# Kernel optimization log

Measured on AMD Instinct MI355X. Metric: run time of the kernel, lower is better.

Reference implementation:

```python
import jax, jax.numpy as jnp
import numpy as np

V, E, U, L = 50000, 512, 20, 9   # vocab, embed dim, user feats, labels
R, S, T = 64, 32, 50             # reviews, sentences/review, tokens/sentence
D = E + U                        # product-encoder input dim


def setup_inputs() -> dict:
    key = jax.random.key(0)
    ks = jax.random.split(key, 16)
    sc = lambda k, shape: (jax.random.normal(k, shape, jnp.float32) * 0.02)
    return {
        "inputs": jax.random.randint(ks[0], (R, S, T), 0, V),
        "user_feats": jax.random.normal(ks[1], (R, U), jnp.float32),
        "embedding": sc(ks[2], (V, E)),
        "w_sent": sc(ks[3], (E, E)), "b_sent": jnp.zeros((E,), jnp.float32),
        "w_rev": sc(ks[4], (E, E)),  "b_rev": jnp.zeros((E,), jnp.float32),
        "w_prod": sc(ks[5], (D, D)), "b_prod": jnp.zeros((D,), jnp.float32),
        "w_rff": sc(ks[6], (D, 1)),  "b_rff": jnp.zeros((1,), jnp.float32),
        "w_pff": sc(ks[7], (D, L)),  "b_pff": jnp.zeros((L,), jnp.float32),
        "user_w": jnp.ones((U,), jnp.float32),
    }


def _masked_mean(x, mask):
    # x: [..., N, F], mask: [..., N] -> [..., F]
    denom = jnp.maximum(mask.sum(-1, keepdims=True), 1.0)
    return (x * mask[..., None]).sum(-2) / denom


def reference(inputs, user_feats, embedding, w_sent, b_sent, w_rev, b_rev,
              w_prod, b_prod, w_rff, b_rff, w_pff, b_pff, user_w):
    dt = embedding.dtype
    tok_mask = (inputs != 0).astype(dt)                      # [R,S,T]
    emb = embedding[inputs]                                  # [R,S,T,E]
    # sentence encoder (DAN): masked mean over tokens + Linear + SELU
    sent_h = jax.nn.selu(_masked_mean(emb, tok_mask) @ w_sent + b_sent)   # [R,S,E]
    # review encoder: masked mean over sentences (r_mask = p.sum(-1) != 0)
    sent_mask = (inputs.sum(-1) != 0).astype(dt)             # [R,S]
    rev_h = jax.nn.selu(_masked_mean(sent_h, sent_mask) @ w_rev + b_rev)  # [R,E]
    # append L2-normalized user feats scaled by learned weights
    norm = jnp.sqrt((user_feats * user_feats).sum(-1, keepdims=True))
    uf = user_feats / jnp.maximum(norm, 1e-12) * user_w      # [R,U]
    p_batch = jnp.concatenate([rev_h, uf], axis=-1)          # [R,D]
    # per-review star head
    r_stars = jax.nn.selu(p_batch @ w_rff + b_rff).squeeze(-1)            # [R]
    # product encoder: plain mean over reviews (no mask) + Linear + SELU
    h_n = jax.nn.selu(p_batch.mean(-2) @ w_prod + b_prod)    # [D]
    p_stars = jax.nn.selu(h_n @ w_pff + b_pff)               # [L]
    return p_stars, r_stars
```

## Files before the change

### kernel.cpp

```cpp
#include <hip/hip_runtime.h>
#include <hip/hip_bf16.h>

#define R_ 64
#define S_ 32
#define T_ 50
#define E_ 512
#define U_ 20
#define D_ 532
#define L_ 9
#define NSENT (R_ * S_)

#define PCHUNK 128
#define NCG 5
#define NKG 5

typedef __attribute__((ext_vector_type(8))) short bf16x8;
typedef __attribute__((ext_vector_type(4))) float f32x4;

__device__ __forceinline__ float selu_f(float x) {
    const float scale = 1.0507009873554805f;
    const float alpha = 1.6732632423543772f;
    return x > 0.0f ? scale * x : scale * alpha * expm1f(x);
}

__global__ __launch_bounds__(256) void k_fused_A(
        const int* __restrict__ inputs,
        const float* __restrict__ emb,
        const float* __restrict__ w_sent,
        const float* __restrict__ w_rev,
        __hip_bfloat16* __restrict__ sent_bf,
        __hip_bfloat16* __restrict__ wT,
        float* __restrict__ smask,
        int* __restrict__ dcount)
{
    const int tid = threadIdx.x;

    if (blockIdx.x >= NSENT) {
        __shared__ float tile[32][33];
        const int b = blockIdx.x - NSENT;
        const int z = b >> 8;
        const float* w = z ? w_rev : w_sent;
        __hip_bfloat16* o = wT + (size_t)z * E_ * E_;
        const int bb = b & 255;
        const int tx = tid & 31, ty = tid >> 5;
        const int k0 = (bb >> 4) * 32, n0 = (bb & 15) * 32;
        #pragma unroll
        for (int i = 0; i < 4; ++i)
            tile[ty + 8 * i][tx] = w[(size_t)(k0 + ty + 8 * i) * E_ + n0 + tx];
        __syncthreads();
        #pragma unroll
        for (int i = 0; i < 4; ++i)
            o[(size_t)(n0 + ty + 8 * i) * E_ + k0 + tx] = __float2bfloat16(tile[tx][ty + 8 * i]);
        return;
    }

    if (blockIdx.x == 0 && tid == 0) *dcount = 0;

    const int sid = blockIdx.x;
    const int base = sid * T_;
    float2 acc = {0.f, 0.f};
    int cnt = 0;
    for (int t = 0; t < T_; ++t) {
        const int tok = inputs[base + t];
        const float m = (tok != 0) ? 1.0f : 0.0f;
        cnt += (tok != 0);
        const float2 v = ((const float2*)(emb + (size_t)tok * E_))[tid];
        acc.x = fmaf(v.x, m, acc.x);
        acc.y = fmaf(v.y, m, acc.y);
    }
    const float inv = 1.0f / fmaxf((float)cnt, 1.0f);
    __hip_bfloat162 h2;
    h2.x = __float2bfloat16(acc.x * inv);
    h2.y = __float2bfloat16(acc.y * inv);
    ((__hip_bfloat162*)(sent_bf + (size_t)sid * E_))[tid] = h2;
    if (tid == 0) smask[sid] = (cnt > 0) ? 1.0f : 0.0f;
}

__global__ __launch_bounds__(256) void k_gemm_sent_mean(
        const __hip_bfloat16* __restrict__ A,
        const __hip_bfloat16* __restrict__ Bt,
        const float* __restrict__ bias,
        const float* __restrict__ smask,
        __hip_bfloat16* __restrict__ mrev)
{
    __shared__ short As[64][40];
    __shared__ short Bs[64][40];
    const int tid  = threadIdx.x;
    const int wid  = tid >> 6;
    const int lane = tid & 63;
    const int wm = wid >> 1, wn = wid & 1;
    const int bm = blockIdx.y * 64, bn = blockIdx.x * 64;
    const int srow = tid >> 2;
    const int soff = (tid & 3) * 8;
    const short* Ag  = (const short*)A;
    const short* Btg = (const short*)Bt;
    const int fr = lane & 15;
    const int kg = (lane >> 4) * 8;
    const int rq = (lane >> 4) * 4;

    f32x4 acc[2][2];
    #pragma unroll
    for (int i = 0; i < 2; ++i)
        #pragma unroll
        for (int j = 0; j < 2; ++j) acc[i][j] = (f32x4){0.f, 0.f, 0.f, 0.f};

    for (int k0 = 0; k0 < E_; k0 += 32) {
        __syncthreads();
        *(bf16x8*)&As[srow][soff] = *(const bf16x8*)&Ag[(size_t)(bm + srow) * E_ + k0 + soff];
        *(bf16x8*)&Bs[srow][soff] = *(const bf16x8*)&Btg[(size_t)(bn + srow) * E_ + k0 + soff];
        __syncthreads();
        bf16x8 af0 = *(const bf16x8*)&As[wm * 32 + fr][kg];
        bf16x8 af1 = *(const bf16x8*)&As[wm * 32 + 16 + fr][kg];
        bf16x8 bf0 = *(const bf16x8*)&Bs[wn * 32 + fr][kg];
        bf16x8 bf1 = *(const bf16x8*)&Bs[wn * 32 + 16 + fr][kg];
        acc[0][0] = __builtin_amdgcn_mfma_f32_16x16x32_bf16(af0, bf0, acc[0][0], 0, 0, 0);
        acc[0][1] = __builtin_amdgcn_mfma_f32_16x16x32_bf16(af0, bf1, acc[0][1], 0, 0, 0);
        acc[1][0] = __builtin_amdgcn_mfma_f32_16x16x32_bf16(af1, bf0, acc[1][0], 0, 0, 0);
        acc[1][1] = __builtin_amdgcn_mfma_f32_16x16x32_bf16(af1, bf1, acc[1][1], 0, 0, 0);
    }

    float m[2][4];
    float msum = 0.f;
    #pragma unroll
    for (int fm = 0; fm < 2; ++fm)
        #pragma unroll
        for (int j = 0; j < 4; ++j) {
            m[fm][j] = smask[bm + wm * 32 + fm * 16 + rq + j];
            msum += m[fm][j];
        }
    float colsum[2];
    #pragma unroll
    for (int fn = 0; fn < 2; ++fn) {
        const float bv = bias[bn + wn * 32 + fn * 16 + fr];
        float s = 0.f;
        #pragma unroll
        for (int fm = 0; fm < 2; ++fm)
            #pragma unroll
            for (int j = 0; j < 4; ++j)
                s = fmaf(selu_f(acc[fm][fn][j] + bv), m[fm][j], s);
        colsum[fn] = s;
    }
    #pragma unroll
    for (int fn = 0; fn < 2; ++fn) {
        colsum[fn] += __shfl_xor(colsum[fn], 16, 64);
        colsum[fn] += __shfl_xor(colsum[fn], 32, 64);
    }
    msum += __shfl_xor(msum, 16, 64);
    msum += __shfl_xor(msum, 32, 64);
    const float inv = 1.0f / fmaxf(msum, 1.0f);
    if (lane < 16) {
        const int g = 2 * blockIdx.y + wm;
        #pragma unroll
        for (int fn = 0; fn < 2; ++fn)
            mrev[(size_t)g * E_ + bn + wn * 32 + fn * 16 + fr] =
                __float2bfloat16(colsum[fn] * inv);
    }
}

__global__ __launch_bounds__(256) void k_gemm_rev(
        const __hip_bfloat16* __restrict__ A,
        const __hip_bfloat16* __restrict__ Bt,
        const float* __restrict__ bias,
        const float* __restrict__ user_feats,
        const float* __restrict__ user_w,
        float* __restrict__ p_batch,
        float* __restrict__ pbar)
{
    __shared__ short As[64][72];
    __shared__ short Bs[64][72];
    __shared__ float cs[2][2][2][16];
    __shared__ float ufl[64][U_];
    const int tid  = threadIdx.x;
    const int wid  = tid >> 6;
    const int lane = tid & 63;
    const int wm = wid >> 1, wn = wid & 1;
    const int bn = blockIdx.x * 64;
    const int fr = lane & 15;
    const int kg = (lane >> 4) * 8;
    const int rq = (lane >> 4) * 4;
    const int srow = tid >> 2;
    const int scol = (tid & 3) * 8;

    if (blockIdx.x == 0 && tid < 64) {
        const int r = tid;
        float ss = 0.f;
        #pragma unroll
        for (int j = 0; j < U_; ++j) {
            const float u = user_feats[r * U_ + j];
            ss = fmaf(u, u, ss);
        }
        const float nrm = fmaxf(sqrtf(ss), 1e-12f);
        #pragma unroll
        for (int j = 0; j < U_; ++j) {
            const float v = user_feats[r * U_ + j] / nrm * user_w[j];
            p_batch[(size_t)r * D_ + E_ + j] = v;
            ufl[r][j] = v;
        }
    }

    const short* Ag  = (const short*)A;
    const short* Btg = (const short*)Bt;

    f32x4 acc[2][2];
    #pragma unroll
    for (int i = 0; i < 2; ++i)
        #pragma unroll
        for (int j = 0; j < 2; ++j) acc[i][j] = (f32x4){0.f, 0.f, 0.f, 0.f};

    for (int k0 = 0; k0 < E_; k0 += 64) {
        __syncthreads();
        *(bf16x8*)&As[srow][scol]      = *(const bf16x8*)&Ag[(size_t)srow * E_ + k0 + scol];
        *(bf16x8*)&As[srow][scol + 32] = *(const bf16x8*)&Ag[(size_t)srow * E_ + k0 + scol + 32];
        *(bf16x8*)&Bs[srow][scol]      = *(const bf16x8*)&Btg[(size_t)(bn + srow) * E_ + k0 + scol];
        *(bf16x8*)&Bs[srow][scol + 32] = *(const bf16x8*)&Btg[(size_t)(bn + srow) * E_ + k0 + scol + 32];
        __syncthreads();
        #pragma unroll
        for (int ks = 0; ks < 64; ks += 32) {
            bf16x8 af0 = *(const bf16x8*)&As[wm * 32 + fr][ks + kg];
            bf16x8 af1 = *(const bf16x8*)&As[wm * 32 + 16 + fr][ks + kg];
            bf16x8 bf0 = *(const bf16x8*)&Bs[wn * 32 + fr][ks + kg];
            bf16x8 bf1 = *(const bf16x8*)&Bs[wn * 32 + 16 + fr][ks + kg];
            acc[0][0] = __builtin_amdgcn_mfma_f32_16x16x32_bf16(af0, bf0, acc[0][0], 0, 0, 0);
            acc[0][1] = __builtin_amdgcn_mfma_f32_16x16x32_bf16(af0, bf1, acc[0][1], 0, 0, 0);
            acc[1][0] = __builtin_amdgcn_mfma_f32_16x16x32_bf16(af1, bf0, acc[1][0], 0, 0, 0);
            acc[1][1] = __builtin_amdgcn_mfma_f32_16x16x32_bf16(af1, bf1, acc[1][1], 0, 0, 0);
        }
    }

    float colsum[2] = {0.f, 0.f};
    #pragma unroll
    for (int fm = 0; fm < 2; ++fm) {
        #pragma unroll
        for (int fn = 0; fn < 2; ++fn) {
            const int col = bn + wn * 32 + fn * 16 + fr;
            const float bv = bias[col];
            #pragma unroll
            for (int j = 0; j < 4; ++j) {
                const int row = wm * 32 + fm * 16 + rq + j;
                const float val = selu_f(acc[fm][fn][j] + bv);
                p_batch[(size_t)row * D_ + col] = val;
                colsum[fn] += val;
            }
        }
    }
    #pragma unroll
    for (int fn = 0; fn < 2; ++fn) {
        colsum[fn] += __shfl_xor(colsum[fn], 16, 64);
        colsum[fn] += __shfl_xor(colsum[fn], 32, 64);
    }
    if (lane < 16) {
        cs[wm][wn][0][fr] = colsum[0];
        cs[wm][wn][1][fr] = colsum[1];
    }
    __syncthreads();
    if (tid < 64) {
        const int wn2 = tid >> 5, fn2 = (tid >> 4) & 1, fr2 = tid & 15;
        const float s = cs[0][wn2][fn2][fr2] + cs[1][wn2][fn2][fr2];
        pbar[bn + wn2 * 32 + fn2 * 16 + fr2] = s * (1.0f / 64.0f);
    }
    if (blockIdx.x == 0 && tid < U_) {
        float s = 0.f;
        #pragma unroll 16
        for (int r = 0; r < 64; ++r) s += ufl[r][tid];
        pbar[E_ + tid] = s * (1.0f / 64.0f);
    }
}

__global__ __launch_bounds__(256) void k_prod_fused(
        const float* __restrict__ pbar_g,
        const float* __restrict__ p_batch,
        const float* __restrict__ w_prod,
        const float* __restrict__ b_prod,
        const float* __restrict__ w_pff,
        const float* __restrict__ b_pff,
        const float* __restrict__ w_rff,
        const float* __restrict__ b_rff,
        float* __restrict__ part,
        int* __restrict__ dcount,
        float* __restrict__ out_p,
        float* __restrict__ out_r)
{
    __shared__ float pb[PCHUNK];
    __shared__ float red[2][PCHUNK];
    const int cg = blockIdx.x, kg = blockIdx.y;
    const int tid = threadIdx.x;
    const int cl = tid & (PCHUNK - 1);
    const int h  = tid >> 7;
    const int k0 = kg * PCHUNK;
    const int klen = min(PCHUNK, D_ - k0);

    if (tid < klen) pb[tid] = pbar_g[k0 + tid];
    __syncthreads();

    const int c = cg * PCHUNK + cl;
    float acc = 0.f;
    if (c < D_) {
        const int jb = h * 64;
        const int je = min(jb + 64, klen);
        for (int j = jb; j < je; ++j)
            acc = fmaf(pb[j], w_prod[(size_t)(k0 + j) * D_ + c], acc);
    }
    red[h][cl] = acc;
    __syncthreads();
    if (h == 0 && c < D_) part[kg * D_ + c] = red[0][cl] + red[1][cl];

    __threadfence();
    __shared__ int is_last;
    if (tid == 0) is_last = (atomicAdd(dcount, 1) == NCG * NKG - 1);
    __syncthreads();
    if (!is_last) return;
    __threadfence();

    __shared__ float hn[D_];
    __shared__ float rred[4][64];
    __shared__ float ppart[L_][28];
    for (int cc = tid; cc < D_; cc += 256) {
        float s = b_prod[cc];
        #pragma unroll
        for (int g = 0; g < NKG; ++g) s += part[g * D_ + cc];
        hn[cc] = selu_f(s);
    }
    __syncthreads();
    if (tid < L_ * 28) {
        const int o = tid / 28, ii = tid % 28;
        float s = 0.f;
        for (int k = ii; k < D_; k += 28)
            s = fmaf(hn[k], w_pff[(size_t)k * L_ + o], s);
        ppart[o][ii] = s;
    }
    {
        const int r = tid & 63, q = tid >> 6;
        float pr = 0.f;
        for (int k = q * 133; k < (q + 1) * 133; ++k)
            pr = fmaf(p_batch[(size_t)r * D_ + k], w_rff[k], pr);
        rred[q][r] = pr;
    }
    __syncthreads();
    if (tid < L_) {
        float s = 0.f;
        #pragma unroll
        for (int ii = 0; ii < 28; ++ii) s += ppart[tid][ii];
        out_p[tid] = selu_f(s + b_pff[tid]);
    }
    if (tid < 64)
        out_r[tid] = selu_f(rred[0][tid] + rred[1][tid] + rred[2][tid] + rred[3][tid]
                            + b_rff[0]);
}

extern "C" void kernel_launch(void* const* d_in, const int* in_sizes, int n_in,
                              void* d_out, int out_size, void* d_ws, size_t ws_size,
                              hipStream_t stream) {
    const int*   inputs     = (const int*)  d_in[0];
    const float* user_feats = (const float*)d_in[1];
    const float* emb        = (const float*)d_in[2];
    const float* w_sent     = (const float*)d_in[3];
    const float* b_sent     = (const float*)d_in[4];
    const float* w_rev      = (const float*)d_in[5];
    const float* b_rev      = (const float*)d_in[6];
    const float* w_prod     = (const float*)d_in[7];
    const float* b_prod     = (const float*)d_in[8];
    const float* w_rff      = (const float*)d_in[9];
    const float* b_rff      = (const float*)d_in[10];
    const float* w_pff      = (const float*)d_in[11];
    const float* b_pff      = (const float*)d_in[12];
    const float* user_w     = (const float*)d_in[13];
    float* out = (float*)d_out;

    float* ws = (float*)d_ws;
    __hip_bfloat16* sent_bf = (__hip_bfloat16*)(ws);
    __hip_bfloat16* wT      = (__hip_bfloat16*)(ws + 524288);
    __hip_bfloat16* mrev    = (__hip_bfloat16*)(ws + 786432);
    float* smask   = ws + 802816;
    float* p_batch = ws + 804864;
    float* part    = ws + 838912;
    float* pbar_ws = ws + 841600;
    int*   dcount  = (int*)(ws + 842144);

    k_fused_A<<<NSENT + 512, 256, 0, stream>>>(inputs, emb, w_sent, w_rev,
                                               sent_bf, wT, smask, dcount);
    k_gemm_sent_mean<<<dim3(E_ / 64, NSENT / 64), 256, 0, stream>>>(
        sent_bf, wT, b_sent, smask, mrev);
    k_gemm_rev<<<dim3(8, 1), 256, 0, stream>>>(
        mrev, wT + (size_t)E_ * E_, b_rev, user_feats, user_w, p_batch, pbar_ws);
    k_prod_fused<<<dim3(NCG, NKG), 256, 0, stream>>>(
        pbar_ws, p_batch, w_prod, b_prod, w_pff, b_pff, w_rff, b_rff,
        part, dcount, out, out + L_);
}
```

Measured before the change: 88.60 us.

## Merge three tail kernels into one persistent kernel with global flag barriers

Fuses the sentence GEMM+mean, review GEMM, and product head into a single 256-block kernel. Stages are ordered by atomic counters in global memory that later blocks spin on, instead of separate kernel launches. This is meant to remove launch overhead and inter-kernel gaps. It relies on all 256 blocks being co-resident to avoid deadlock, and it adds spin-wait and fence costs.

```diff
diff --git a/kernel.cpp b/kernel.cpp
--- a/kernel.cpp
+++ b/kernel.cpp
@@ -14,6 +14,10 @@
 #define NCG 5
 #define NKG 5
 
+#define FG1 0
+#define FG2 16
+#define FD  32
+
 typedef __attribute__((ext_vector_type(8))) short bf16x8;
 typedef __attribute__((ext_vector_type(4))) float f32x4;
 
@@ -21,6 +25,11 @@
     const float scale = 1.0507009873554805f;
     const float alpha = 1.6732632423543772f;
     return x > 0.0f ? scale * x : scale * alpha * expm1f(x);
+}
+
+__device__ __forceinline__ void spin_until(const int* f, int target) {
+    while (__hip_atomic_load(f, __ATOMIC_RELAXED, __HIP_MEMORY_SCOPE_AGENT) < target)
+        __builtin_amdgcn_s_sleep(2);
 }
 
 __global__ __launch_bounds__(256) void k_fused_A(
@@ -31,7 +40,7 @@
         __hip_bfloat16* __restrict__ sent_bf,
         __hip_bfloat16* __restrict__ wT,
         float* __restrict__ smask,
-        int* __restrict__ dcount)
+        int* __restrict__ fl)
 {
     const int tid = threadIdx.x;
 
@@ -54,7 +63,7 @@
         return;
     }
 
-    if (blockIdx.x == 0 && tid == 0) *dcount = 0;
+    if (blockIdx.x == 0 && tid < 48) fl[tid] = 0;
 
     const int sid = blockIdx.x;
     const int base = sid * T_;
@@ -76,275 +85,282 @@
     if (tid == 0) smask[sid] = (cnt > 0) ? 1.0f : 0.0f;
 }
 
-__global__ __launch_bounds__(256) void k_gemm_sent_mean(
-        const __hip_bfloat16* __restrict__ A,
-        const __hip_bfloat16* __restrict__ Bt,
-        const float* __restrict__ bias,
+__global__ __launch_bounds__(256) void k_tail(
+        const __hip_bfloat16* __restrict__ sent_bf,
+        const __hip_bfloat16* __restrict__ wT,
+        const float* __restrict__ b_sent,
         const float* __restrict__ smask,
-        __hip_bfloat16* __restrict__ mrev)
-{
-    __shared__ short As[64][40];
-    __shared__ short Bs[64][40];
-    const int tid  = threadIdx.x;
-    const int wid  = tid >> 6;
-    const int lane = tid & 63;
-    const int wm = wid >> 1, wn = wid & 1;
-    const int bm = blockIdx.y * 64, bn = blockIdx.x * 64;
-    const int srow = tid >> 2;
-    const int soff = (tid & 3) * 8;
-    const short* Ag  = (const short*)A;
-    const short* Btg = (const short*)Bt;
-    const int fr = lane & 15;
-    const int kg = (lane >> 4) * 8;
-    const int rq = (lane >> 4) * 4;
-
-    f32x4 acc[2][2];
-    #pragma unroll
-    for (int i = 0; i < 2; ++i)
-        #pragma unroll
-        for (int j = 0; j < 2; ++j) acc[i][j] = (f32x4){0.f, 0.f, 0.f, 0.f};
-
-    for (int k0 = 0; k0 < E_; k0 += 32) {
-        __syncthreads();
-        *(bf16x8*)&As[srow][soff] = *(const bf16x8*)&Ag[(size_t)(bm + srow) * E_ + k0 + soff];
-        *(bf16x8*)&Bs[srow][soff] = *(const bf16x8*)&Btg[(size_t)(bn + srow) * E_ + k0 + soff];
-        __syncthreads();
-        bf16x8 af0 = *(const bf16x8*)&As[wm * 32 + fr][kg];
-        bf16x8 af1 = *(const bf16x8*)&As[wm * 32 + 16 + fr][kg];
-        bf16x8 bf0 = *(const bf16x8*)&Bs[wn * 32 + fr][kg];
-        bf16x8 bf1 = *(const bf16x8*)&Bs[wn * 32 + 16 + fr][kg];
-        acc[0][0] = __builtin_amdgcn_mfma_f32_16x16x32_bf16(af0, bf0, acc[0][0], 0, 0, 0);
-        acc[0][1] = __builtin_amdgcn_mfma_f32_16x16x32_bf16(af0, bf1, acc[0][1], 0, 0, 0);
-        acc[1][0] = __builtin_amdgcn_mfma_f32_16x16x32_bf16(af1, bf0, acc[1][0], 0, 0, 0);
-        acc[1][1] = __builtin_amdgcn_mfma_f32_16x16x32_bf16(af1, bf1, acc[1][1], 0, 0, 0);
-    }
-
-    float m[2][4];
-    float msum = 0.f;
-    #pragma unroll
-    for (int fm = 0; fm < 2; ++fm)
-        #pragma unroll
-        for (int j = 0; j < 4; ++j) {
-            m[fm][j] = smask[bm + wm * 32 + fm * 16 + rq + j];
-            msum += m[fm][j];
-        }
-    float colsum[2];
-    #pragma unroll
-    for (int fn = 0; fn < 2; ++fn) {
-        const float bv = bias[bn + wn * 32 + fn * 16 + fr];
-        float s = 0.f;
-        #pragma unroll
-        for (int fm = 0; fm < 2; ++fm)
-            #pragma unroll
-            for (int j = 0; j < 4; ++j)
-                s = fmaf(selu_f(acc[fm][fn][j] + bv), m[fm][j], s);
-        colsum[fn] = s;
-    }
-    #pragma unroll
-    for (int fn = 0; fn < 2; ++fn) {
-        colsum[fn] += __shfl_xor(colsum[fn], 16, 64);
-        colsum[fn] += __shfl_xor(colsum[fn], 32, 64);
-    }
-    msum += __shfl_xor(msum, 16, 64);
-    msum += __shfl_xor(msum, 32, 64);
-    const float inv = 1.0f / fmaxf(msum, 1.0f);
-    if (lane < 16) {
-        const int g = 2 * blockIdx.y + wm;
-        #pragma unroll
-        for (int fn = 0; fn < 2; ++fn)
-            mrev[(size_t)g * E_ + bn + wn * 32 + fn * 16 + fr] =
-                __float2bfloat16(colsum[fn] * inv);
-    }
-}
-
-__global__ __launch_bounds__(256) void k_gemm_rev(
-        const __hip_bfloat16* __restrict__ A,
-        const __hip_bfloat16* __restrict__ Bt,
-        const float* __restrict__ bias,
+        const float* __restrict__ b_rev,
         const float* __restrict__ user_feats,
         const float* __restrict__ user_w,
-        float* __restrict__ p_batch,
-        float* __restrict__ pbar)
-{
-    __shared__ short As[64][72];
-    __shared__ short Bs[64][72];
-    __shared__ float cs[2][2][2][16];
-    __shared__ float ufl[64][U_];
-    const int tid  = threadIdx.x;
-    const int wid  = tid >> 6;
-    const int lane = tid & 63;
-    const int wm = wid >> 1, wn = wid & 1;
-    const int bn = blockIdx.x * 64;
-    const int fr = lane & 15;
-    const int kg = (lane >> 4) * 8;
-    const int rq = (lane >> 4) * 4;
-    const int srow = tid >> 2;
-    const int scol = (tid & 3) * 8;
-
-    if (blockIdx.x == 0 && tid < 64) {
-        const int r = tid;
-        float ss = 0.f;
-        #pragma unroll
-        for (int j = 0; j < U_; ++j) {
-            const float u = user_feats[r * U_ + j];
-            ss = fmaf(u, u, ss);
-        }
-        const float nrm = fmaxf(sqrtf(ss), 1e-12f);
-        #pragma unroll
-        for (int j = 0; j < U_; ++j) {
-            const float v = user_feats[r * U_ + j] / nrm * user_w[j];
-            p_batch[(size_t)r * D_ + E_ + j] = v;
-            ufl[r][j] = v;
-        }
-    }
-
-    const short* Ag  = (const short*)A;
-    const short* Btg = (const short*)Bt;
-
-    f32x4 acc[2][2];
-    #pragma unroll
-    for (int i = 0; i < 2; ++i)
-        #pragma unroll
-        for (int j = 0; j < 2; ++j) acc[i][j] = (f32x4){0.f, 0.f, 0.f, 0.f};
-
-    for (int k0 = 0; k0 < E_; k0 += 64) {
-        __syncthreads();
-        *(bf16x8*)&As[srow][scol]      = *(const bf16x8*)&Ag[(size_t)srow * E_ + k0 + scol];
-        *(bf16x8*)&As[srow][scol + 32] = *(const bf16x8*)&Ag[(size_t)srow * E_ + k0 + scol + 32];
-        *(bf16x8*)&Bs[srow][scol]      = *(const bf16x8*)&Btg[(size_t)(bn + srow) * E_ + k0 + scol];
-        *(bf16x8*)&Bs[srow][scol + 32] = *(const bf16x8*)&Btg[(size_t)(bn + srow) * E_ + k0 + scol + 32];
-        __syncthreads();
-        #pragma unroll
-        for (int ks = 0; ks < 64; ks += 32) {
-            bf16x8 af0 = *(const bf16x8*)&As[wm * 32 + fr][ks + kg];
-            bf16x8 af1 = *(const bf16x8*)&As[wm * 32 + 16 + fr][ks + kg];
-            bf16x8 bf0 = *(const bf16x8*)&Bs[wn * 32 + fr][ks + kg];
-            bf16x8 bf1 = *(const bf16x8*)&Bs[wn * 32 + 16 + fr][ks + kg];
-            acc[0][0] = __builtin_amdgcn_mfma_f32_16x16x32_bf16(af0, bf0, acc[0][0], 0, 0, 0);
-            acc[0][1] = __builtin_amdgcn_mfma_f32_16x16x32_bf16(af0, bf1, acc[0][1], 0, 0, 0);
-            acc[1][0] = __builtin_amdgcn_mfma_f32_16x16x32_bf16(af1, bf0, acc[1][0], 0, 0, 0);
-            acc[1][1] = __builtin_amdgcn_mfma_f32_16x16x32_bf16(af1, bf1, acc[1][1], 0, 0, 0);
-        }
-    }
-
-    float colsum[2] = {0.f, 0.f};
-    #pragma unroll
-    for (int fm = 0; fm < 2; ++fm) {
-        #pragma unroll
-        for (int fn = 0; fn < 2; ++fn) {
-            const int col = bn + wn * 32 + fn * 16 + fr;
-            const float bv = bias[col];
-            #pragma unroll
-            for (int j = 0; j < 4; ++j) {
-                const int row = wm * 32 + fm * 16 + rq + j;
-                const float val = selu_f(acc[fm][fn][j] + bv);
-                p_batch[(size_t)row * D_ + col] = val;
-                colsum[fn] += val;
-            }
-        }
-    }
-    #pragma unroll
-    for (int fn = 0; fn < 2; ++fn) {
-        colsum[fn] += __shfl_xor(colsum[fn], 16, 64);
-        colsum[fn] += __shfl_xor(colsum[fn], 32, 64);
-    }
-    if (lane < 16) {
-        cs[wm][wn][0][fr] = colsum[0];
-        cs[wm][wn][1][fr] = colsum[1];
-    }
-    __syncthreads();
-    if (tid < 64) {
-        const int wn2 = tid >> 5, fn2 = (tid >> 4) & 1, fr2 = tid & 15;
-        const float s = cs[0][wn2][fn2][fr2] + cs[1][wn2][fn2][fr2];
-        pbar[bn + wn2 * 32 + fn2 * 16 + fr2] = s * (1.0f / 64.0f);
-    }
-    if (blockIdx.x == 0 && tid < U_) {
-        float s = 0.f;
-        #pragma unroll 16
-        for (int r = 0; r < 64; ++r) s += ufl[r][tid];
-        pbar[E_ + tid] = s * (1.0f / 64.0f);
-    }
-}
-
-__global__ __launch_bounds__(256) void k_prod_fused(
-        const float* __restrict__ pbar_g,
-        const float* __restrict__ p_batch,
         const float* __restrict__ w_prod,
         const float* __restrict__ b_prod,
         const float* __restrict__ w_pff,
         const float* __restrict__ b_pff,
         const float* __restrict__ w_rff,
         const float* __restrict__ b_rff,
+        __hip_bfloat16* __restrict__ mrev,
+        float* __restrict__ p_batch,
+        float* __restrict__ pbar,
         float* __restrict__ part,
-        int* __restrict__ dcount,
+        int* __restrict__ fl,
         float* __restrict__ out_p,
         float* __restrict__ out_r)
 {
-    __shared__ float pb[PCHUNK];
-    __shared__ float red[2][PCHUNK];
-    const int cg = blockIdx.x, kg = blockIdx.y;
+    __shared__ __align__(16) char smem[24576];
     const int tid = threadIdx.x;
-    const int cl = tid & (PCHUNK - 1);
-    const int h  = tid >> 7;
-    const int k0 = kg * PCHUNK;
-    const int klen = min(PCHUNK, D_ - k0);
-
-    if (tid < klen) pb[tid] = pbar_g[k0 + tid];
-    __syncthreads();
-
-    const int c = cg * PCHUNK + cl;
-    float acc = 0.f;
-    if (c < D_) {
-        const int jb = h * 64;
-        const int je = min(jb + 64, klen);
-        for (int j = jb; j < je; ++j)
-            acc = fmaf(pb[j], w_prod[(size_t)(k0 + j) * D_ + c], acc);
-    }
-    red[h][cl] = acc;
-    __syncthreads();
-    if (h == 0 && c < D_) part[kg * D_ + c] = red[0][cl] + red[1][cl];
-
-    __threadfence();
-    __shared__ int is_last;
-    if (tid == 0) is_last = (atomicAdd(dcount, 1) == NCG * NKG - 1);
-    __syncthreads();
-    if (!is_last) return;
-    __threadfence();
-
-    __shared__ float hn[D_];
-    __shared__ float rred[4][64];
-    __shared__ float ppart[L_][28];
-    for (int cc = tid; cc < D_; cc += 256) {
-        float s = b_prod[cc];
-        #pragma unroll
-        for (int g = 0; g < NKG; ++g) s += part[g * D_ + cc];
-        hn[cc] = selu_f(s);
+    const int b   = blockIdx.x;
+    const int wid  = tid >> 6;
+    const int lane = tid & 63;
+    const int wm = wid >> 1, wn = wid & 1;
+    const int fr = lane & 15;
+    const int kg = (lane >> 4) * 8;
+    const int rq = (lane >> 4) * 4;
+    const int srow = tid >> 2;
+    const int soff = (tid & 3) * 8;
+
+    {
+        short (*As)[40] = (short(*)[40])smem;
+        short (*Bs)[40] = (short(*)[40])(smem + 5120);
+        const int bm = (b >> 3) * 64, bn = (b & 7) * 64;
+        const short* Ag  = (const short*)sent_bf;
+        const short* Btg = (const short*)wT;
+
+        f32x4 acc[2][2];
+        #pragma unroll
+        for (int i = 0; i < 2; ++i)
+            #pragma unroll
+            for (int j = 0; j < 2; ++j) acc[i][j] = (f32x4){0.f, 0.f, 0.f, 0.f};
+
+        for (int k0 = 0; k0 < E_; k0 += 32) {
+            __syncthreads();
+            *(bf16x8*)&As[srow][soff] = *(const bf16x8*)&Ag[(size_t)(bm + srow) * E_ + k0 + soff];
+            *(bf16x8*)&Bs[srow][soff] = *(const bf16x8*)&Btg[(size_t)(bn + srow) * E_ + k0 + soff];
+            __syncthreads();
+            bf16x8 af0 = *(const bf16x8*)&As[wm * 32 + fr][kg];
+            bf16x8 af1 = *(const bf16x8*)&As[wm * 32 + 16 + fr][kg];
+            bf16x8 bf0 = *(const bf16x8*)&Bs[wn * 32 + fr][kg];
+            bf16x8 bf1 = *(const bf16x8*)&Bs[wn * 32 + 16 + fr][kg];
+            acc[0][0] = __builtin_amdgcn_mfma_f32_16x16x32_bf16(af0, bf0, acc[0][0], 0, 0, 0);
+            acc[0][1] = __builtin_amdgcn_mfma_f32_16x16x32_bf16(af0, bf1, acc[0][1], 0, 0, 0);
+            acc[1][0] = __builtin_amdgcn_mfma_f32_16x16x32_bf16(af1, bf0, acc[1][0], 0, 0, 0);
+            acc[1][1] = __builtin_amdgcn_mfma_f32_16x16x32_bf16(af1, bf1, acc[1][1], 0, 0, 0);
+        }
+
+        float m[2][4];
+        float msum = 0.f;
+        #pragma unroll
+        for (int fm = 0; fm < 2; ++fm)
+            #pragma unroll
+            for (int j = 0; j < 4; ++j) {
+                m[fm][j] = smask[bm + wm * 32 + fm * 16 + rq + j];
+                msum += m[fm][j];
+            }
+        float colsum[2];
+        #pragma unroll
+        for (int fn = 0; fn < 2; ++fn) {
+            const float bv = b_sent[bn + wn * 32 + fn * 16 + fr];
+            float s = 0.f;
+            #pragma unroll
+            for (int fm = 0; fm < 2; ++fm)
+                #pragma unroll
+                for (int j = 0; j < 4; ++j)
+                    s = fmaf(selu_f(acc[fm][fn][j] + bv), m[fm][j], s);
+            colsum[fn] = s;
+        }
+        #pragma unroll
+        for (int fn = 0; fn < 2; ++fn) {
+            colsum[fn] += __shfl_xor(colsum[fn], 16, 64);
+            colsum[fn] += __shfl_xor(colsum[fn], 32, 64);
+        }
+        msum += __shfl_xor(msum, 16, 64);
+        msum += __shfl_xor(msum, 32, 64);
+        const float inv = 1.0f / fmaxf(msum, 1.0f);
+        if (lane < 16) {
+            const int g = 2 * (b >> 3) + wm;
+            #pragma unroll
+            for (int fn = 0; fn < 2; ++fn)
+                mrev[(size_t)g * E_ + bn + wn * 32 + fn * 16 + fr] =
+                    __float2bfloat16(colsum[fn] * inv);
+        }
     }
     __syncthreads();
-    if (tid < L_ * 28) {
-        const int o = tid / 28, ii = tid % 28;
-        float s = 0.f;
-        for (int k = ii; k < D_; k += 28)
-            s = fmaf(hn[k], w_pff[(size_t)k * L_ + o], s);
-        ppart[o][ii] = s;
+    __threadfence();
+    if (tid == 0) atomicAdd(&fl[FG1], 1);
+
+    if (b >= NCG * NKG) return;
+
+    if (b < 8) {
+        if (tid == 0) spin_until(&fl[FG1], 256);
+        __syncthreads();
+        __threadfence();
+
+        short (*As2)[72] = (short(*)[72])smem;
+        short (*Bs2)[72] = (short(*)[72])(smem + 9216);
+        float (*cs)[2][2][16] = (float(*)[2][2][16])(smem + 18432);
+        float (*ufl)[U_] = (float(*)[U_])(smem + 18944);
+        const int bn = b * 64;
+        const int scol = (tid & 3) * 8;
+
+        if (b == 0 && tid < 64) {
+            const int r = tid;
+            float ss = 0.f;
+            #pragma unroll
+            for (int j = 0; j < U_; ++j) {
+                const float u = user_feats[r * U_ + j];
+                ss = fmaf(u, u, ss);
+            }
+            const float nrm = fmaxf(sqrtf(ss), 1e-12f);
+            #pragma unroll
+            for (int j = 0; j < U_; ++j) {
+                const float v = user_feats[r * U_ + j] / nrm * user_w[j];
+                p_batch[(size_t)r * D_ + E_ + j] = v;
+                ufl[r][j] = v;
+            }
+        }
+
+        const short* Ag  = (const short*)mrev;
+        const short* Btg = (const short*)(wT + (size_t)E_ * E_);
+
+        f32x4 acc[2][2];
+        #pragma unroll
+        for (int i = 0; i < 2; ++i)
+            #pragma unroll
+            for (int j = 0; j < 2; ++j) acc[i][j] = (f32x4){0.f, 0.f, 0.f, 0.f};
+
+        for (int k0 = 0; k0 < E_; k0 += 64) {
+            __syncthreads();
+            *(bf16x8*)&As2[srow][scol]      = *(const bf16x8*)&Ag[(size_t)srow * E_ + k0 + scol];
+            *(bf16x8*)&As2[srow][scol + 32] = *(const bf16x8*)&Ag[(size_t)srow * E_ + k0 + scol + 32];
+            *(bf16x8*)&Bs2[srow][scol]      = *(const bf16x8*)&Btg[(size_t)(bn + srow) * E_ + k0 + scol];
+            *(bf16x8*)&Bs2[srow][scol + 32] = *(const bf16x8*)&Btg[(size_t)(bn + srow) * E_ + k0 + scol + 32];
+            __syncthreads();
+            #pragma unroll
+            for (int ks = 0; ks < 64; ks += 32) {
+                bf16x8 af0 = *(const bf16x8*)&As2[wm * 32 + fr][ks + kg];
+                bf16x8 af1 = *(const bf16x8*)&As2[wm * 32 + 16 + fr][ks + kg];
+                bf16x8 bf0 = *(const bf16x8*)&Bs2[wn * 32 + fr][ks + kg];
+                bf16x8 bf1 = *(const bf16x8*)&Bs2[wn * 32 + 16 + fr][ks + kg];
+                acc[0][0] = __builtin_amdgcn_mfma_f32_16x16x32_bf16(af0, bf0, acc[0][0], 0, 0, 0);
+                acc[0][1] = __builtin_amdgcn_mfma_f32_16x16x32_bf16(af0, bf1, acc[0][1], 0, 0, 0);
+                acc[1][0] = __builtin_amdgcn_mfma_f32_16x16x32_bf16(af1, bf0, acc[1][0], 0, 0, 0);
+                acc[1][1] = __builtin_amdgcn_mfma_f32_16x16x32_bf16(af1, bf1, acc[1][1], 0, 0, 0);
+            }
+        }
+
+        float colsum[2] = {0.f, 0.f};
+        #pragma unroll
+        for (int fm = 0; fm < 2; ++fm) {
+            #pragma unroll
+            for (int fn = 0; fn < 2; ++fn) {
+                const int col = bn + wn * 32 + fn * 16 + fr;
+                const float bv = b_rev[col];
+                #pragma unroll
+                for (int j = 0; j < 4; ++j) {
+                    const int row = wm * 32 + fm * 16 + rq + j;
+                    const float val = selu_f(acc[fm][fn][j] + bv);
+                    p_batch[(size_t)row * D_ + col] = val;
+                    colsum[fn] += val;
+                }
+            }
+        }
+        #pragma unroll
+        for (int fn = 0; fn < 2; ++fn) {
+            colsum[fn] += __shfl_xor(colsum[fn], 16, 64);
+            colsum[fn] += __shfl_xor(colsum[fn], 32, 64);
+        }
+        if (lane < 16) {
+            cs[wm][wn][0][fr] = colsum[0];
+            cs[wm][wn][1][fr] = colsum[1];
+        }
+        __syncthreads();
+        if (tid < 64) {
+            const int wn2 = tid >> 5, fn2 = (tid >> 4) & 1, fr2 = tid & 15;
+            const float s = cs[0][wn2][fn2][fr2] + cs[1][wn2][fn2][fr2];
+            pbar[bn + wn2 * 32 + fn2 * 16 + fr2] = s * (1.0f / 64.0f);
+        }
+        if (b == 0 && tid < U_) {
+            float s = 0.f;
+            #pragma unroll 16
+            for (int r = 0; r < 64; ++r) s += ufl[r][tid];
+            pbar[E_ + tid] = s * (1.0f / 64.0f);
+        }
+        __syncthreads();
+        __threadfence();
+        if (tid == 0) atomicAdd(&fl[FG2], 1);
     }
+
     {
-        const int r = tid & 63, q = tid >> 6;
-        float pr = 0.f;
-        for (int k = q * 133; k < (q + 1) * 133; ++k)
-            pr = fmaf(p_batch[(size_t)r * D_ + k], w_rff[k], pr);
-        rred[q][r] = pr;
+        if (tid == 0) spin_until(&fl[FG2], 8);
+        __syncthreads();
+        __threadfence();
+
+        float* pb = (float*)smem;
+        float (*red)[PCHUNK] = (float(*)[PCHUNK])(smem + 512);
+        const int cg = b % NCG, kgrp = b / NCG;
+        const int cl = tid & (PCHUNK - 1);
+        const int h  = tid >> 7;
+        const int k0 = kgrp * PCHUNK;
+        const int klen = min(PCHUNK, D_ - k0);
+
+        if (tid < klen) pb[tid] = pbar[k0 + tid];
+        __syncthreads();
+
+        const int c = cg * PCHUNK + cl;
+        float acc = 0.f;
+        if (c < D_) {
+            const int jb = h * 64;
+            const int je = min(jb + 64, klen);
+            for (int j = jb; j < je; ++j)
+                acc = fmaf(pb[j], w_prod[(size_t)(k0 + j) * D_ + c], acc);
+        }
+        red[h][cl] = acc;
+        __syncthreads();
+        if (h == 0 && c < D_) part[kgrp * D_ + c] = red[0][cl] + red[1][cl];
+
+        __syncthreads();
+        __threadfence();
+        __shared__ int is_last;
+        if (tid == 0) is_last = (atomicAdd(&fl[FD], 1) == NCG * NKG - 1);
+        __syncthreads();
+        if (!is_last) return;
+        __threadfence();
+
+        float* hn = (float*)(smem + 1536);
+        float (*rred)[64] = (float(*)[64])(smem + 3712);
+        float (*ppart)[28] = (float(*)[28])(smem + 4736);
+        for (int cc = tid; cc < D_; cc += 256) {
+            float s = b_prod[cc];
+            #pragma unroll
+            for (int g = 0; g < NKG; ++g) s += part[g * D_ + cc];
+            hn[cc] = selu_f(s);
+        }
+        __syncthreads();
+        if (tid < L_ * 28) {
+            const int o = tid / 28, ii = tid % 28;
+            float s = 0.f;
+            for (int k = ii; k < D_; k += 28)
+                s = fmaf(hn[k], w_pff[(size_t)k * L_ + o], s);
+            ppart[o][ii] = s;
+        }
+        {
+            const int r = tid & 63, q = tid >> 6;
+            float pr = 0.f;
+            for (int k = q * 133; k < (q + 1) * 133; ++k)
+                pr = fmaf(p_batch[(size_t)r * D_ + k], w_rff[k], pr);
+            rred[q][r] = pr;
+        }
+        __syncthreads();
+        if (tid < L_) {
+            float s = 0.f;
+            #pragma unroll
+            for (int ii = 0; ii < 28; ++ii) s += ppart[tid][ii];
+            out_p[tid] = selu_f(s + b_pff[tid]);
+        }
+        if (tid < 64)
+            out_r[tid] = selu_f(rred[0][tid] + rred[1][tid] + rred[2][tid] + rred[3][tid]
+                                + b_rff[0]);
     }
-    __syncthreads();
-    if (tid < L_) {
-        float s = 0.f;
-        #pragma unroll
-        for (int ii = 0; ii < 28; ++ii) s += ppart[tid][ii];
-        out_p[tid] = selu_f(s + b_pff[tid]);
-    }
-    if (tid < 64)
-        out_r[tid] = selu_f(rred[0][tid] + rred[1][tid] + rred[2][tid] + rred[3][tid]
-                            + b_rff[0]);
 }
 
 extern "C" void kernel_launch(void* const* d_in, const int* in_sizes, int n_in,
@@ -374,15 +390,12 @@
     float* p_batch = ws + 804864;
     float* part    = ws + 838912;
     float* pbar_ws = ws + 841600;
-    int*   dcount  = (int*)(ws + 842144);
+    int*   flags   = (int*)(ws + 842144);
 
     k_fused_A<<<NSENT + 512, 256, 0, stream>>>(inputs, emb, w_sent, w_rev,
-                                               sent_bf, wT, smask, dcount);
-    k_gemm_sent_mean<<<dim3(E_ / 64, NSENT / 64), 256, 0, stream>>>(
-        sent_bf, wT, b_sent, smask, mrev);
-    k_gemm_rev<<<dim3(8, 1), 256, 0, stream>>>(
-        mrev, wT + (size_t)E_ * E_, b_rev, user_feats, user_w, p_batch, pbar_ws);
-    k_prod_fused<<<dim3(NCG, NKG), 256, 0, stream>>>(
-        pbar_ws, p_batch, w_prod, b_prod, w_pff, b_pff, w_rff, b_rff,
-        part, dcount, out, out + L_);
+                                               sent_bf, wT, smask, flags);
+    k_tail<<<256, 256, 0, stream>>>(
+        sent_bf, wT, b_sent, smask, b_rev, user_feats, user_w,
+        w_prod, b_prod, w_pff, b_pff, w_rff, b_rff,
+        mrev, p_batch, pbar_ws, part, flags, out, out + L_);
 }
```

Measured after the change: 107.0 us. 1.21x slower.
